# Kernel optimization log

Hardware: AMD Instinct MI355X
Metric: run time of the kernel (lower is better)

Reference implementation:

```python
import jax, jax.numpy as jnp
import numpy as np

T, N, E = 8, 5000, 160000
IN_DIM, HID, H = 64, 128, 8
D = HID // H  # head dim = 16
NC = 2
EPS = 1e-5


def layer_norm(x, g, b):
    mu = jnp.mean(x, axis=-1, keepdims=True)
    var = jnp.mean((x - mu) ** 2, axis=-1, keepdims=True)
    return (x - mu) / jnp.sqrt(var + EPS) * g + b


def setup_inputs() -> dict:
    key = jax.random.key(0)
    ks = jax.random.split(key, 24)
    p = {}
    p["x"] = jax.random.normal(ks[0], (T, N, IN_DIM), dtype=jnp.float32)
    p["edge_index"] = jax.random.randint(ks[1], (T, 2, E), 0, N, dtype=jnp.int32)
    p["noise"] = jax.random.normal(ks[2], (N, HID), dtype=jnp.float32)
    def w(k, shape, fan_in):
        return jax.random.normal(k, shape, dtype=jnp.float32) * (1.0 / np.sqrt(fan_in))
    p["W_proj"] = w(ks[3], (IN_DIM, HID), IN_DIM)
    p["b_proj"] = jnp.zeros((HID,), jnp.float32)
    p["W_gat"] = w(ks[4], (HID, HID), HID)
    p["a_src"] = w(ks[5], (H, D), D)
    p["a_dst"] = w(ks[6], (H, D), D)
    p["b_gat"] = jnp.zeros((HID,), jnp.float32)
    p["g1"] = jnp.ones((HID,), jnp.float32)
    p["be1"] = jnp.zeros((HID,), jnp.float32)
    p["W_qkv"] = w(ks[7], (3 * HID, HID), HID)
    p["b_qkv"] = jnp.zeros((3 * HID,), jnp.float32)
    p["W_o"] = w(ks[8], (HID, HID), HID)
    p["b_o"] = jnp.zeros((HID,), jnp.float32)
    p["g2"] = jnp.ones((HID,), jnp.float32)
    p["be2"] = jnp.zeros((HID,), jnp.float32)
    p["Wc1"] = w(ks[9], (HID, HID), HID)
    p["bc1"] = jnp.zeros((HID,), jnp.float32)
    p["gc"] = jnp.ones((HID,), jnp.float32)
    p["bec"] = jnp.zeros((HID,), jnp.float32)
    p["Wc2"] = w(ks[10], (HID, NC), HID)
    p["bc2"] = jnp.array([0.0, 0.1], jnp.float32)
    return p


def reference(x, edge_index, noise, W_proj, b_proj, W_gat, a_src, a_dst, b_gat,
              g1, be1, W_qkv, b_qkv, W_o, b_o, g2, be2,
              Wc1, bc1, gc, bec, Wc2, bc2):
    # per-timestep projection + ReLU: [T, N, HID]
    h = jax.nn.relu(x @ W_proj + b_proj)

    loop = jnp.arange(N, dtype=edge_index.dtype)

    def gat(h_t, ei):  # h_t: [N, HID], ei: [2, E]
        src = jnp.concatenate([ei[0], loop])  # add self loops
        dst = jnp.concatenate([ei[1], loop])
        xh = (h_t @ W_gat).reshape(N, H, D)          # [N, H, D]
        a_s = jnp.sum(xh * a_src, axis=-1)           # [N, H]
        a_d = jnp.sum(xh * a_dst, axis=-1)           # [N, H]
        e = jax.nn.leaky_relu(a_s[src] + a_d[dst], 0.2)  # [E', H]
        m = jax.ops.segment_max(e, dst, num_segments=N)
        ex = jnp.exp(e - m[dst])
        s = jax.ops.segment_sum(ex, dst, num_segments=N)
        alpha = ex / (s[dst] + 1e-16)                # segment softmax per dst/head
        out = jax.ops.segment_sum(xh[src] * alpha[..., None], dst, num_segments=N)
        return out.reshape(N, HID) + b_gat

    feats = jax.vmap(gat)(h, edge_index)             # [T, N, HID]
    nf = jnp.transpose(feats, (1, 0, 2))             # [N, T, HID] (node = batch)

    nrm = layer_norm(nf, g1, be1)
    qkv = nrm @ W_qkv.T + b_qkv                      # [N, T, 3*HID]
    q, k, v = jnp.split(qkv, 3, axis=-1)
    def heads(t):
        return t.reshape(N, T, H, D).transpose(0, 2, 1, 3)  # [N, H, T, D]
    q, k, v = heads(q), heads(k), heads(v)
    scores = jnp.einsum('nhqd,nhkd->nhqk', q, k) / jnp.sqrt(jnp.float32(D))
    attn = jax.nn.softmax(scores, axis=-1)
    ta = jnp.einsum('nhqk,nhkd->nhqd', attn, v)
    ta = ta.transpose(0, 2, 1, 3).reshape(N, T, HID) @ W_o.T + b_o

    fused = layer_norm(nf + ta, g2, be2)
    emb = fused[:, -1, :]                            # [N, HID]

    node_ids = jnp.arange(N, dtype=jnp.float32) / N
    div = jnp.sin(node_ids * 6.28) * 0.1             # [N]
    emb = emb + div[:, None] + noise * 0.05          # eval noise scale

    h1 = emb @ Wc1 + bc1
    h1 = jax.nn.gelu(layer_norm(h1, gc, bec), approximate=False)
    logits = h1 @ Wc2 + bc2                          # [N, 2]
    sinu = jnp.sin(jnp.arange(N, dtype=jnp.float32) * 0.5) * 0.2
    logits = logits.at[:, 1].add(sinu)
    return emb, logits
```

## Files before the change

### kernel.cpp

```cpp
#include <hip/hip_runtime.h>
#include <math.h>

#define T 8
#define N 5000
#define E 160000
#define EN (E + N)
#define IN_DIM 64
#define HID 128
#define H 8
#define D 16
#define NC 2
#define MT 32
#define NBF 4
#define NRR 8
#define NCHK 32
#define NHCH 32
#define RSZ ((N + NRR - 1) / NRR)
#define CSZ ((EN + NCHK - 1) / NCHK)

__device__ __forceinline__ float leaky(float e) { return (e >= 0.0f) ? e : 0.2f * e; }

__global__ __launch_bounds__(256) void k_pg(const float* __restrict__ x,
                                            const float* __restrict__ Wp,
                                            const float* __restrict__ bp,
                                            const float* __restrict__ Wg,
                                            const float* __restrict__ asrc,
                                            const float* __restrict__ adst,
                                            float* __restrict__ xh,
                                            float* __restrict__ a_s,
                                            float* __restrict__ a_d,
                                            int* __restrict__ cursor) {
    __shared__ float xt[MT][IN_DIM];
    __shared__ float ht[MT][HID + 1];
    int row0 = blockIdx.x * MT;
    int tid = threadIdx.x;

    {
        int gi = blockIdx.x * 256 + tid;
        if (gi < T * N) cursor[gi] = 0;
    }

    for (int idx = tid; idx < MT * IN_DIM; idx += 256) {
        int r = idx >> 6, k = idx & 63;
        xt[r][k] = x[(size_t)(row0 + r) * IN_DIM + k];
    }
    __syncthreads();

    int cg = tid & 31;
    int rg = tid >> 5;
    int c0 = cg * 4, r0 = rg * 4;

    {
        float4 b4 = *(const float4*)(bp + c0);
        float a00=b4.x,a01=b4.y,a02=b4.z,a03=b4.w;
        float a10=b4.x,a11=b4.y,a12=b4.z,a13=b4.w;
        float a20=b4.x,a21=b4.y,a22=b4.z,a23=b4.w;
        float a30=b4.x,a31=b4.y,a32=b4.z,a33=b4.w;
        for (int k = 0; k < IN_DIM; ++k) {
            float4 w = *(const float4*)(Wp + (size_t)k * HID + c0);
            float x0 = xt[r0 + 0][k], x1 = xt[r0 + 1][k];
            float x2 = xt[r0 + 2][k], x3 = xt[r0 + 3][k];
            a00 += x0*w.x; a01 += x0*w.y; a02 += x0*w.z; a03 += x0*w.w;
            a10 += x1*w.x; a11 += x1*w.y; a12 += x1*w.z; a13 += x1*w.w;
            a20 += x2*w.x; a21 += x2*w.y; a22 += x2*w.z; a23 += x2*w.w;
            a30 += x3*w.x; a31 += x3*w.y; a32 += x3*w.z; a33 += x3*w.w;
        }
        ht[r0+0][c0+0]=fmaxf(a00,0.f); ht[r0+0][c0+1]=fmaxf(a01,0.f);
        ht[r0+0][c0+2]=fmaxf(a02,0.f); ht[r0+0][c0+3]=fmaxf(a03,0.f);
        ht[r0+1][c0+0]=fmaxf(a10,0.f); ht[r0+1][c0+1]=fmaxf(a11,0.f);
        ht[r0+1][c0+2]=fmaxf(a12,0.f); ht[r0+1][c0+3]=fmaxf(a13,0.f);
        ht[r0+2][c0+0]=fmaxf(a20,0.f); ht[r0+2][c0+1]=fmaxf(a21,0.f);
        ht[r0+2][c0+2]=fmaxf(a22,0.f); ht[r0+2][c0+3]=fmaxf(a23,0.f);
        ht[r0+3][c0+0]=fmaxf(a30,0.f); ht[r0+3][c0+1]=fmaxf(a31,0.f);
        ht[r0+3][c0+2]=fmaxf(a32,0.f); ht[r0+3][c0+3]=fmaxf(a33,0.f);
    }
    __syncthreads();

    float a00=0,a01=0,a02=0,a03=0, a10=0,a11=0,a12=0,a13=0;
    float a20=0,a21=0,a22=0,a23=0, a30=0,a31=0,a32=0,a33=0;
    for (int k = 0; k < HID; ++k) {
        float4 w = *(const float4*)(Wg + (size_t)k * HID + c0);
        float h0 = ht[r0 + 0][k], h1 = ht[r0 + 1][k];
        float h2 = ht[r0 + 2][k], h3 = ht[r0 + 3][k];
        a00 += h0*w.x; a01 += h0*w.y; a02 += h0*w.z; a03 += h0*w.w;
        a10 += h1*w.x; a11 += h1*w.y; a12 += h1*w.z; a13 += h1*w.w;
        a20 += h2*w.x; a21 += h2*w.y; a22 += h2*w.z; a23 += h2*w.w;
        a30 += h3*w.x; a31 += h3*w.y; a32 += h3*w.z; a33 += h3*w.w;
    }
    {
        float4 v;
        v.x=a00; v.y=a01; v.z=a02; v.w=a03;
        *(float4*)(xh + (size_t)(row0 + r0 + 0) * HID + c0) = v;
        v.x=a10; v.y=a11; v.z=a12; v.w=a13;
        *(float4*)(xh + (size_t)(row0 + r0 + 1) * HID + c0) = v;
        v.x=a20; v.y=a21; v.z=a22; v.w=a23;
        *(float4*)(xh + (size_t)(row0 + r0 + 2) * HID + c0) = v;
        v.x=a30; v.y=a31; v.z=a32; v.w=a33;
        *(float4*)(xh + (size_t)(row0 + r0 + 3) * HID + c0) = v;
    }
    __syncthreads();
    ht[r0+0][c0+0]=a00; ht[r0+0][c0+1]=a01; ht[r0+0][c0+2]=a02; ht[r0+0][c0+3]=a03;
    ht[r0+1][c0+0]=a10; ht[r0+1][c0+1]=a11; ht[r0+1][c0+2]=a12; ht[r0+1][c0+3]=a13;
    ht[r0+2][c0+0]=a20; ht[r0+2][c0+1]=a21; ht[r0+2][c0+2]=a22; ht[r0+2][c0+3]=a23;
    ht[r0+3][c0+0]=a30; ht[r0+3][c0+1]=a31; ht[r0+3][c0+2]=a32; ht[r0+3][c0+3]=a33;
    __syncthreads();

    {
        int r = tid >> 3, hh = tid & 7;
        float s1 = 0.0f, s2 = 0.0f;
        #pragma unroll
        for (int d = 0; d < D; ++d) {
            float v = ht[r][hh * D + d];
            s1 += v * asrc[hh * D + d];
            s2 += v * adst[hh * D + d];
        }
        a_s[(size_t)(row0 + r) * H + hh] = s1;
        a_d[(size_t)(row0 + r) * H + hh] = s2;
    }
}

__global__ void k_tr(const float* __restrict__ W_qkv, const float* __restrict__ W_o,
                     float* __restrict__ WTq, float* __restrict__ WoT) {
    int idx = blockIdx.x * 256 + threadIdx.x;
    if (idx < 384 * 128) {
        int j = idx >> 7, c = idx & 127;
        WTq[c * 384 + j] = W_qkv[idx];
    } else if (idx < 384 * 128 + 128 * 128) {
        int r = idx - 384 * 128;
        int j = r >> 7, k = r & 127;
        WoT[k * 128 + j] = W_o[r];
    }
}

__global__ __launch_bounds__(256) void k_hist(const int* __restrict__ ei,
                                              int* __restrict__ cursor) {
    __shared__ int hist[N];
    int t = blockIdx.x >> 5;
    int chunk = blockIdx.x & 31;
    int tid = threadIdx.x;

    for (int i = tid; i < N; i += 256) hist[i] = 0;
    __syncthreads();

    const int CS = (EN + NHCH - 1) / NHCH;
    int i0 = chunk * CS;
    int i1 = (i0 + CS < EN) ? i0 + CS : EN;
    const int* drow = ei + (size_t)(2 * t + 1) * E;
    for (int i = i0 + tid; i < i1; i += 256) {
        int d = (i < E) ? drow[i] : (i - E);
        atomicAdd(&hist[d], 1);
    }
    __syncthreads();

    int* cur = cursor + t * N;
    for (int i = tid; i < N; i += 256) {
        int c = hist[i];
        if (c) atomicAdd(&cur[i], c);
    }
}

__global__ void k_scan(int* __restrict__ cursor, int* __restrict__ offs) {
    __shared__ int part[256];
    int t = blockIdx.x;
    int tid = threadIdx.x;
    const int CH = 20;
    int begin = tid * CH;
    int sum = 0;
    for (int k = 0; k < CH; ++k) {
        int i = begin + k;
        if (i < N) sum += cursor[t * N + i];
    }
    part[tid] = sum;
    __syncthreads();
    if (tid == 0) {
        int run = 0;
        for (int i = 0; i < 256; ++i) { int v = part[i]; part[i] = run; run += v; }
        offs[t * (N + 1) + N] = run;
    }
    __syncthreads();
    int run = part[tid];
    for (int k = 0; k < CH; ++k) {
        int i = begin + k;
        if (i < N) {
            int cnt = cursor[t * N + i];
            offs[t * (N + 1) + i] = run;
            cursor[t * N + i] = run;
            run += cnt;
        }
    }
}

__global__ __launch_bounds__(256) void k_scatter(const int* __restrict__ ei,
                                                 int* __restrict__ cursor,
                                                 int* __restrict__ csr_src) {
    int idx = blockIdx.x;
    int g = idx & 63;
    int c = idx >> 6;
    int t = g >> 3;
    int r = g & 7;
    int lo = r * RSZ;
    int hi = (lo + RSZ < N) ? lo + RSZ : N;
    int i0 = c * CSZ;
    int i1 = (i0 + CSZ < EN) ? i0 + CSZ : EN;

    const int* srow = ei + (size_t)(2 * t) * E;
    const int* drow = srow + E;
    int* cur = cursor + t * N;
    int* csb = csr_src + (size_t)t * EN;

    for (int i = i0 + threadIdx.x; i < i1; i += 256) {
        int s, d;
        if (i < E) { d = drow[i]; s = srow[i]; }
        else       { s = d = i - E; }
        if (d >= lo && d < hi) {
            int pos = atomicAdd(&cur[d], 1);
            csb[pos] = s;
        }
    }
}

__global__ __launch_bounds__(128) void k_aggc(
        const int* __restrict__ offs, const int* __restrict__ csr_src,
        const float* __restrict__ a_s, const float* __restrict__ a_d,
        const float* __restrict__ xh, const float* __restrict__ b_gat,
        const float* __restrict__ g1, const float* __restrict__ be1,
        float* __restrict__ nrm, float* __restrict__ xlast_g) {
    int b = blockIdx.x;
    int t = b & 7;
    int dst = b >> 3;
    int tid = threadIdx.x;

    int o0 = offs[t * (N + 1) + dst];
    int o1 = offs[t * (N + 1) + dst + 1];
    int deg = o1 - o0;
    const int* esrc = csr_src + (size_t)t * EN + o0;
    const float* as_b = a_s + (size_t)t * N * H;
    const float* ad_b = a_d + (size_t)t * N * H;
    const float* xh_b = xh + (size_t)t * N * HID;

    __shared__ float ws_s[2][H];
    __shared__ float pacc[2][HID];
    __shared__ float red[128];

    int el = tid >> 5;
    int cg = tid & 31;
    int hg = cg >> 2;
    float adh = ad_b[dst * H + hg];

    float4 acc = {0.0f, 0.0f, 0.0f, 0.0f};
    float wpart = 0.0f;

    #pragma unroll 4
    for (int ej = el; ej < deg; ej += 4) {
        int src = esrc[ej];
        float w = expf(leaky(as_b[src * H + hg] + adh));
        wpart += w;
        float4 v = *(const float4*)(xh_b + (size_t)src * HID + (cg << 2));
        acc.x += w * v.x; acc.y += w * v.y;
        acc.z += w * v.z; acc.w += w * v.w;
    }

    wpart += __shfl_xor(wpart, 32);
    acc.x += __shfl_xor(acc.x, 32);
    acc.y += __shfl_xor(acc.y, 32);
    acc.z += __shfl_xor(acc.z, 32);
    acc.w += __shfl_xor(acc.w, 32);
    if (!(tid & 32)) {
        if ((cg & 3) == 0) ws_s[tid >> 6][hg] = wpart;
        *(float4*)&pacc[tid >> 6][cg << 2] = acc;
    }
    __syncthreads();

    float wsum = ws_s[0][tid >> 4] + ws_s[1][tid >> 4];
    float val = (pacc[0][tid] + pacc[1][tid]) / (wsum + 1e-16f);

    float v = val + b_gat[tid];
    red[tid] = v;
    __syncthreads();
    if (tid < 64) {
        float s = red[tid] + red[tid + 64];
        #pragma unroll
        for (int m = 1; m < 64; m <<= 1) s += __shfl_xor(s, m);
        if (tid == 0) red[0] = s;
    }
    __syncthreads();
    float mu = red[0] * (1.0f / HID);
    __syncthreads();
    float dv = v - mu;
    red[tid] = dv * dv;
    __syncthreads();
    if (tid < 64) {
        float s = red[tid] + red[tid + 64];
        #pragma unroll
        for (int m = 1; m < 64; m <<= 1) s += __shfl_xor(s, m);
        if (tid == 0) red[0] = s;
    }
    __syncthreads();
    float rstd = rsqrtf(red[0] * (1.0f / HID) + 1e-5f);

    nrm[(size_t)(dst * T + t) * HID + tid] = dv * rstd * g1[tid] + be1[tid];
    if (t == T - 1) xlast_g[(size_t)dst * HID + tid] = v;
}

__global__ __launch_bounds__(256) void k_fuse(
        const float* __restrict__ nrm,
        const float* __restrict__ WTq,
        const float* __restrict__ b_qkv,
        const float* __restrict__ xlast_g,
        const float* __restrict__ WoT,
        const float* __restrict__ b_o,
        const float* __restrict__ g2, const float* __restrict__ be2,
        const float* __restrict__ noise, float* __restrict__ out) {
    __shared__ float at[NBF * T][HID];
    __shared__ float ql[NBF][HID];
    __shared__ float ws[2][8][384];
    float* ta_s = &at[0][0];

    int n0 = blockIdx.x * NBF;
    int tid = threadIdx.x;
    int cg = tid & 31, rg = tid >> 5;
    int c0 = cg * 4, r0 = rg * 4;
    int u = rg >> 1;
    int lane = tid & 63, wv = tid >> 6;

    auto stage = [&](int kc, int buf) {
        const float* g = WTq + (size_t)kc * 3072 + wv * 768 + (lane << 2);
        float* l = &ws[buf][0][0] + wv * 768;
        #pragma unroll
        for (int j = 0; j < 3; ++j) {
            __builtin_amdgcn_global_load_lds(
                (const __attribute__((address_space(1))) void*)(g + j * 256),
                (__attribute__((address_space(3))) void*)(l + j * 256),
                16, 0, 0);
        }
    };

    {
        const float* srcp = nrm + (size_t)n0 * T * HID;
        for (int idx = tid; idx < NBF * T * 32; idx += 256) {
            int r = idx >> 5, c4 = (idx & 31) << 2;
            *(float4*)&at[r][c4] = *(const float4*)(srcp + (size_t)r * HID + c4);
        }
    }
    stage(0, 0);

    float ka[4][4], va[4][4], qa[4];
    {
        float4 bk = *(const float4*)(b_qkv + 128 + c0);
        float4 bv = *(const float4*)(b_qkv + 256 + c0);
        #pragma unroll
        for (int i = 0; i < 4; ++i) {
            ka[i][0] = bk.x; ka[i][1] = bk.y; ka[i][2] = bk.z; ka[i][3] = bk.w;
            va[i][0] = bv.x; va[i][1] = bv.y; va[i][2] = bv.z; va[i][3] = bv.w;
        }
        if (rg < 4) {
            float4 bq = *(const float4*)(b_qkv + c0);
            qa[0] = bq.x; qa[1] = bq.y; qa[2] = bq.z; qa[3] = bq.w;
        } else {
            qa[0] = qa[1] = qa[2] = qa[3] = 0.0f;
        }
    }
    __syncthreads();

    const float* atq = at[(rg & 3) * T + (T - 1)];

    int cur = 0;
    for (int kc = 0; kc < 16; ++kc) {
        if (kc < 15) stage(kc + 1, cur ^ 1);

        #pragma unroll
        for (int kk = 0; kk < 8; kk += 4) {
            int k = kc * 8 + kk;
            float4 e0 = *(const float4*)&at[r0 + 0][k];
            float4 e1 = *(const float4*)&at[r0 + 1][k];
            float4 e2 = *(const float4*)&at[r0 + 2][k];
            float4 e3 = *(const float4*)&at[r0 + 3][k];
            float e0a[4] = {e0.x, e0.y, e0.z, e0.w};
            float e1a[4] = {e1.x, e1.y, e1.z, e1.w};
            float e2a[4] = {e2.x, e2.y, e2.z, e2.w};
            float e3a[4] = {e3.x, e3.y, e3.z, e3.w};
            float eqa[4] = {0.f, 0.f, 0.f, 0.f};
            if (rg < 4) {
                float4 eq = *(const float4*)&atq[k];
                eqa[0] = eq.x; eqa[1] = eq.y; eqa[2] = eq.z; eqa[3] = eq.w;
            }
            #pragma unroll
            for (int j = 0; j < 4; ++j) {
                float4 wk = *(const float4*)&ws[cur][kk + j][128 + c0];
                float4 wv4 = *(const float4*)&ws[cur][kk + j][256 + c0];
                float x0 = e0a[j], x1 = e1a[j], x2 = e2a[j], x3 = e3a[j];
                ka[0][0] += x0*wk.x; ka[0][1] += x0*wk.y; ka[0][2] += x0*wk.z; ka[0][3] += x0*wk.w;
                ka[1][0] += x1*wk.x; ka[1][1] += x1*wk.y; ka[1][2] += x1*wk.z; ka[1][3] += x1*wk.w;
                ka[2][0] += x2*wk.x; ka[2][1] += x2*wk.y; ka[2][2] += x2*wk.z; ka[2][3] += x2*wk.w;
                ka[3][0] += x3*wk.x; ka[3][1] += x3*wk.y; ka[3][2] += x3*wk.z; ka[3][3] += x3*wk.w;
                va[0][0] += x0*wv4.x; va[0][1] += x0*wv4.y; va[0][2] += x0*wv4.z; va[0][3] += x0*wv4.w;
                va[1][0] += x1*wv4.x; va[1][1] += x1*wv4.y; va[1][2] += x1*wv4.z; va[1][3] += x1*wv4.w;
                va[2][0] += x2*wv4.x; va[2][1] += x2*wv4.y; va[2][2] += x2*wv4.z; va[2][3] += x2*wv4.w;
                va[3][0] += x3*wv4.x; va[3][1] += x3*wv4.y; va[3][2] += x3*wv4.z; va[3][3] += x3*wv4.w;
                if (rg < 4) {
                    float4 wq = *(const float4*)&ws[cur][kk + j][c0];
                    float xq = eqa[j];
                    qa[0] += xq*wq.x; qa[1] += xq*wq.y; qa[2] += xq*wq.z; qa[3] += xq*wq.w;
                }
            }
        }
        __syncthreads();
        cur ^= 1;
    }

    if (rg < 4) {
        float4 q4; q4.x = qa[0]; q4.y = qa[1]; q4.z = qa[2]; q4.w = qa[3];
        *(float4*)&ql[rg][c0] = q4;
    }
    __syncthreads();

    float p0, p1, p2, p3;
    {
        float4 q4 = *(const float4*)&ql[u][c0];
        float ps[4];
        #pragma unroll
        for (int i = 0; i < 4; ++i) {
            float s = q4.x * ka[i][0] + q4.y * ka[i][1]
                    + q4.z * ka[i][2] + q4.w * ka[i][3];
            s += __shfl_xor(s, 1);
            s += __shfl_xor(s, 2);
            ps[i] = s * 0.25f;
        }
        float mx = fmaxf(fmaxf(ps[0], ps[1]), fmaxf(ps[2], ps[3]));
        mx = fmaxf(mx, __shfl_xor(mx, 32));
        float e0 = expf(ps[0] - mx), e1 = expf(ps[1] - mx);
        float e2 = expf(ps[2] - mx), e3 = expf(ps[3] - mx);
        float ssum = e0 + e1 + e2 + e3;
        ssum += __shfl_xor(ssum, 32);
        float inv = 1.0f / ssum;
        p0 = (e0 * va[0][0] + e1 * va[1][0] + e2 * va[2][0] + e3 * va[3][0]) * inv;
        p1 = (e0 * va[0][1] + e1 * va[1][1] + e2 * va[2][1] + e3 * va[3][1]) * inv;
        p2 = (e0 * va[0][2] + e1 * va[1][2] + e2 * va[2][2] + e3 * va[3][2]) * inv;
        p3 = (e0 * va[0][3] + e1 * va[1][3] + e2 * va[2][3] + e3 * va[3][3]) * inv;
        p0 += __shfl_xor(p0, 32);
        p1 += __shfl_xor(p1, 32);
        p2 += __shfl_xor(p2, 32);
        p3 += __shfl_xor(p3, 32);
    }
    if (!(tid & 32)) {
        float4 t4; t4.x = p0; t4.y = p1; t4.z = p2; t4.w = p3;
        *(float4*)&ta_s[u * 128 + c0] = t4;
    }
    __syncthreads();

    {
        int uu = tid >> 6, c = tid & 63;
        int n = n0 + uu;
        float o0 = b_o[c], o1 = b_o[c + 64];
        const float* tar = ta_s + uu * 128;
        #pragma unroll 8
        for (int k = 0; k < HID; k += 4) {
            float t0 = tar[k], t1 = tar[k+1], t2 = tar[k+2], t3 = tar[k+3];
            o0 += t0 * WoT[(size_t)(k+0)*128 + c]  + t1 * WoT[(size_t)(k+1)*128 + c]
                + t2 * WoT[(size_t)(k+2)*128 + c]  + t3 * WoT[(size_t)(k+3)*128 + c];
            o1 += t0 * WoT[(size_t)(k+0)*128 + c+64] + t1 * WoT[(size_t)(k+1)*128 + c+64]
                + t2 * WoT[(size_t)(k+2)*128 + c+64] + t3 * WoT[(size_t)(k+3)*128 + c+64];
        }
        float xa = xlast_g[(size_t)n * HID + c];
        float xb = xlast_g[(size_t)n * HID + c + 64];
        float x2a = xa + o0, x2b = xb + o1;
        float s = x2a + x2b, qs = x2a * x2a + x2b * x2b;
        #pragma unroll
        for (int m = 1; m < 64; m <<= 1) {
            s  += __shfl_xor(s, m);
            qs += __shfl_xor(qs, m);
        }
        float mu = s * (1.0f / HID);
        float var = qs * (1.0f / HID) - mu * mu;
        float rstd = rsqrtf(var + 1e-5f);
        float dv = sinf(((float)n / (float)N) * 6.28f) * 0.1f;
        out[(size_t)n * HID + c] =
            (x2a - mu) * rstd * g2[c] + be2[c] + dv
            + noise[(size_t)n * HID + c] * 0.05f;
        out[(size_t)n * HID + c + 64] =
            (x2b - mu) * rstd * g2[c + 64] + be2[c + 64] + dv
            + noise[(size_t)n * HID + c + 64] * 0.05f;
    }
}

__global__ __launch_bounds__(256) void k_cls(const float* __restrict__ emb,
                                             const float* __restrict__ Wc1,
                                             const float* __restrict__ bc1,
                                             const float* __restrict__ gc,
                                             const float* __restrict__ bec,
                                             const float* __restrict__ Wc2,
                                             const float* __restrict__ bc2,
                                             float* __restrict__ out) {
    __shared__ float et[MT][HID];
    __shared__ float h1t[MT][HID + 1];
    int row0 = blockIdx.x * MT;
    int tid = threadIdx.x;

    for (int idx = tid; idx < MT * HID; idx += 256) {
        int r = idx >> 7, c = idx & 127;
        int row = row0 + r;
        et[r][c] = (row < N) ? emb[(size_t)row * HID + c] : 0.0f;
    }
    __syncthreads();

    {
        int cg = tid & 31, rg = tid >> 5;
        int c0 = cg * 4, r0 = rg * 4;
        float4 b4 = *(const float4*)(bc1 + c0);
        float a00=b4.x,a01=b4.y,a02=b4.z,a03=b4.w;
        float a10=b4.x,a11=b4.y,a12=b4.z,a13=b4.w;
        float a20=b4.x,a21=b4.y,a22=b4.z,a23=b4.w;
        float a30=b4.x,a31=b4.y,a32=b4.z,a33=b4.w;
        for (int k = 0; k < HID; ++k) {
            float4 w = *(const float4*)(Wc1 + (size_t)k * HID + c0);
            float e0 = et[r0 + 0][k], e1 = et[r0 + 1][k];
            float e2 = et[r0 + 2][k], e3 = et[r0 + 3][k];
            a00 += e0*w.x; a01 += e0*w.y; a02 += e0*w.z; a03 += e0*w.w;
            a10 += e1*w.x; a11 += e1*w.y; a12 += e1*w.z; a13 += e1*w.w;
            a20 += e2*w.x; a21 += e2*w.y; a22 += e2*w.z; a23 += e2*w.w;
            a30 += e3*w.x; a31 += e3*w.y; a32 += e3*w.z; a33 += e3*w.w;
        }
        h1t[r0+0][c0+0]=a00; h1t[r0+0][c0+1]=a01; h1t[r0+0][c0+2]=a02; h1t[r0+0][c0+3]=a03;
        h1t[r0+1][c0+0]=a10; h1t[r0+1][c0+1]=a11; h1t[r0+1][c0+2]=a12; h1t[r0+1][c0+3]=a13;
        h1t[r0+2][c0+0]=a20; h1t[r0+2][c0+1]=a21; h1t[r0+2][c0+2]=a22; h1t[r0+2][c0+3]=a23;
        h1t[r0+3][c0+0]=a30; h1t[r0+3][c0+1]=a31; h1t[r0+3][c0+2]=a32; h1t[r0+3][c0+3]=a33;
    }
    __syncthreads();

    {
        int r = tid >> 3, l = tid & 7;
        float p = 0.0f;
        #pragma unroll
        for (int k = 0; k < 16; ++k) p += h1t[r][l + 8 * k];
        #pragma unroll
        for (int m = 1; m < 8; m <<= 1) p += __shfl_xor(p, m);
        float mu = p * (1.0f / HID);
        float v = 0.0f;
        #pragma unroll
        for (int k = 0; k < 16; ++k) { float d = h1t[r][l + 8 * k] - mu; v += d * d; }
        #pragma unroll
        for (int m = 1; m < 8; m <<= 1) v += __shfl_xor(v, m);
        float rstd = rsqrtf(v * (1.0f / HID) + 1e-5f);
        #pragma unroll
        for (int k = 0; k < 16; ++k) {
            int c = l + 8 * k;
            float lnv = (h1t[r][c] - mu) * rstd * gc[c] + bec[c];
            h1t[r][c] = 0.5f * lnv * (1.0f + erff(lnv * 0.70710678118f));
        }
    }
    __syncthreads();

    if (tid < MT * NC) {
        int r = tid >> 1, j = tid & 1;
        int row = row0 + r;
        if (row < N) {
            float acc = bc2[j];
            #pragma unroll 8
            for (int c = 0; c < HID; ++c) acc += h1t[r][c] * Wc2[c * NC + j];
            if (j == 1) acc += sinf((float)row * 0.5f) * 0.2f;
            out[(size_t)N * HID + (size_t)row * NC + j] = acc;
        }
    }
}

extern "C" void kernel_launch(void* const* d_in, const int* in_sizes, int n_in,
                              void* d_out, int out_size, void* d_ws, size_t ws_size,
                              hipStream_t stream) {
    const float* x      = (const float*)d_in[0];
    const int*   ei     = (const int*)d_in[1];
    const float* noise  = (const float*)d_in[2];
    const float* W_proj = (const float*)d_in[3];
    const float* b_proj = (const float*)d_in[4];
    const float* W_gat  = (const float*)d_in[5];
    const float* a_src  = (const float*)d_in[6];
    const float* a_dst  = (const float*)d_in[7];
    const float* b_gat  = (const float*)d_in[8];
    const float* g1     = (const float*)d_in[9];
    const float* be1    = (const float*)d_in[10];
    const float* W_qkv  = (const float*)d_in[11];
    const float* b_qkv  = (const float*)d_in[12];
    const float* W_o    = (const float*)d_in[13];
    const float* b_o    = (const float*)d_in[14];
    const float* g2     = (const float*)d_in[15];
    const float* be2    = (const float*)d_in[16];
    const float* Wc1    = (const float*)d_in[17];
    const float* bc1    = (const float*)d_in[18];
    const float* gc     = (const float*)d_in[19];
    const float* bec    = (const float*)d_in[20];
    const float* Wc2    = (const float*)d_in[21];
    const float* bc2    = (const float*)d_in[22];
    float* out = (float*)d_out;

    float* xh     = (float*)d_ws;
    float* nrm    = xh + 5120000;
    float* a_s    = nrm + 5120000;
    float* a_d    = a_s + 320000;
    int*   offs    = (int*)(a_d + 320000);
    int*   cursor  = offs + 40008;
    int*   csr_src = cursor + 40000;
    float* WTq    = (float*)(csr_src + 1320000);
    float* WoT    = WTq + 49152;
    float* xlastg = WoT + 16384;

    k_tr<<<(384 * 128 + 128 * 128 + 255) / 256, 256, 0, stream>>>(W_qkv, W_o, WTq, WoT);

    k_pg<<<T * N / MT, 256, 0, stream>>>(x, W_proj, b_proj, W_gat, a_src, a_dst,
                                         xh, a_s, a_d, cursor);

    k_hist<<<T * NHCH, 256, 0, stream>>>(ei, cursor);
    k_scan<<<T, 256, 0, stream>>>(cursor, offs);
    k_scatter<<<64 * NCHK, 256, 0, stream>>>(ei, cursor, csr_src);

    k_aggc<<<T * N, 128, 0, stream>>>(offs, csr_src, a_s, a_d, xh,
                                      b_gat, g1, be1, nrm, xlastg);

    k_fuse<<<N / NBF, 256, 0, stream>>>(nrm, WTq, b_qkv, xlastg, WoT, b_o,
                                        g2, be2, noise, out);

    k_cls<<<(N + MT - 1) / MT, 256, 0, stream>>>(out, Wc1, bc1, gc, bec, Wc2, bc2, out);
}
```

Before: 349.6 us.

## Merge weight transpose, projection and edge histogram into one front kernel

Three independent front-stage kernels (weight transpose, projection+GAT linear, destination histogram) are combined into a single launch whose blocks branch on block index into the three roles, sharing a union shared-memory buffer. The cursor zeroing that k_pg used to do is replaced with a hipMemsetAsync before the launch, since histogram blocks now run concurrently with the former zeroing blocks. This removes two launches and lets the atomic histogram overlap the GEMM work. In exchange, every block reserves the largest shared-memory footprint, which may lower occupancy for the transpose and projection blocks, and a memset node is added.

```diff
diff --git a/kernel.cpp b/kernel.cpp
--- a/kernel.cpp
+++ b/kernel.cpp
@@ -18,27 +18,74 @@
 #define RSZ ((N + NRR - 1) / NRR)
 #define CSZ ((EN + NCHK - 1) / NCHK)
 
+#define NB_HIST (T * NHCH)
+#define NB_TR   256
+#define NB_PG   (T * N / MT)
+
 __device__ __forceinline__ float leaky(float e) { return (e >= 0.0f) ? e : 0.2f * e; }
 
-__global__ __launch_bounds__(256) void k_pg(const float* __restrict__ x,
-                                            const float* __restrict__ Wp,
-                                            const float* __restrict__ bp,
-                                            const float* __restrict__ Wg,
-                                            const float* __restrict__ asrc,
-                                            const float* __restrict__ adst,
-                                            float* __restrict__ xh,
-                                            float* __restrict__ a_s,
-                                            float* __restrict__ a_d,
-                                            int* __restrict__ cursor) {
-    __shared__ float xt[MT][IN_DIM];
-    __shared__ float ht[MT][HID + 1];
-    int row0 = blockIdx.x * MT;
+__global__ __launch_bounds__(256) void k_front(
+        const float* __restrict__ x,
+        const float* __restrict__ Wp,
+        const float* __restrict__ bp,
+        const float* __restrict__ Wg,
+        const float* __restrict__ asrc,
+        const float* __restrict__ adst,
+        float* __restrict__ xh,
+        float* __restrict__ a_s,
+        float* __restrict__ a_d,
+        const float* __restrict__ W_qkv,
+        const float* __restrict__ W_o,
+        float* __restrict__ WTq,
+        float* __restrict__ WoT,
+        const int* __restrict__ ei,
+        int* __restrict__ cursor) {
+    __shared__ float smem[6272];
+    int bid = blockIdx.x;
     int tid = threadIdx.x;
 
-    {
-        int gi = blockIdx.x * 256 + tid;
-        if (gi < T * N) cursor[gi] = 0;
-    }
+    if (bid < NB_HIST) {
+        int* hist = (int*)smem;
+        int t = bid >> 5;
+        int chunk = bid & 31;
+
+        for (int i = tid; i < N; i += 256) hist[i] = 0;
+        __syncthreads();
+
+        const int CS = (EN + NHCH - 1) / NHCH;
+        int i0 = chunk * CS;
+        int i1 = (i0 + CS < EN) ? i0 + CS : EN;
+        const int* drow = ei + (size_t)(2 * t + 1) * E;
+        for (int i = i0 + tid; i < i1; i += 256) {
+            int d = (i < E) ? drow[i] : (i - E);
+            atomicAdd(&hist[d], 1);
+        }
+        __syncthreads();
+
+        int* cur = cursor + t * N;
+        for (int i = tid; i < N; i += 256) {
+            int c = hist[i];
+            if (c) atomicAdd(&cur[i], c);
+        }
+        return;
+    }
+
+    if (bid < NB_HIST + NB_TR) {
+        int idx = (bid - NB_HIST) * 256 + tid;
+        if (idx < 384 * 128) {
+            int j = idx >> 7, c = idx & 127;
+            WTq[c * 384 + j] = W_qkv[idx];
+        } else if (idx < 384 * 128 + 128 * 128) {
+            int r = idx - 384 * 128;
+            int j = r >> 7, k = r & 127;
+            WoT[k * 128 + j] = W_o[r];
+        }
+        return;
+    }
+
+    float (*xt)[IN_DIM] = (float (*)[IN_DIM])smem;
+    float (*ht)[HID + 1] = (float (*)[HID + 1])(smem + MT * IN_DIM);
+    int row0 = (bid - NB_HIST - NB_TR) * MT;
 
     for (int idx = tid; idx < MT * IN_DIM; idx += 256) {
         int r = idx >> 6, k = idx & 63;
@@ -116,46 +163,6 @@
         }
         a_s[(size_t)(row0 + r) * H + hh] = s1;
         a_d[(size_t)(row0 + r) * H + hh] = s2;
-    }
-}
-
-__global__ void k_tr(const float* __restrict__ W_qkv, const float* __restrict__ W_o,
-                     float* __restrict__ WTq, float* __restrict__ WoT) {
-    int idx = blockIdx.x * 256 + threadIdx.x;
-    if (idx < 384 * 128) {
-        int j = idx >> 7, c = idx & 127;
-        WTq[c * 384 + j] = W_qkv[idx];
-    } else if (idx < 384 * 128 + 128 * 128) {
-        int r = idx - 384 * 128;
-        int j = r >> 7, k = r & 127;
-        WoT[k * 128 + j] = W_o[r];
-    }
-}
-
-__global__ __launch_bounds__(256) void k_hist(const int* __restrict__ ei,
-                                              int* __restrict__ cursor) {
-    __shared__ int hist[N];
-    int t = blockIdx.x >> 5;
-    int chunk = blockIdx.x & 31;
-    int tid = threadIdx.x;
-
-    for (int i = tid; i < N; i += 256) hist[i] = 0;
-    __syncthreads();
-
-    const int CS = (EN + NHCH - 1) / NHCH;
-    int i0 = chunk * CS;
-    int i1 = (i0 + CS < EN) ? i0 + CS : EN;
-    const int* drow = ei + (size_t)(2 * t + 1) * E;
-    for (int i = i0 + tid; i < i1; i += 256) {
-        int d = (i < E) ? drow[i] : (i - E);
-        atomicAdd(&hist[d], 1);
-    }
-    __syncthreads();
-
-    int* cur = cursor + t * N;
-    for (int i = tid; i < N; i += 256) {
-        int c = hist[i];
-        if (c) atomicAdd(&cur[i], c);
     }
 }
 
@@ -602,12 +609,12 @@
     float* WoT    = WTq + 49152;
     float* xlastg = WoT + 16384;
 
-    k_tr<<<(384 * 128 + 128 * 128 + 255) / 256, 256, 0, stream>>>(W_qkv, W_o, WTq, WoT);
-
-    k_pg<<<T * N / MT, 256, 0, stream>>>(x, W_proj, b_proj, W_gat, a_src, a_dst,
-                                         xh, a_s, a_d, cursor);
-
-    k_hist<<<T * NHCH, 256, 0, stream>>>(ei, cursor);
+    hipMemsetAsync(cursor, 0, 40000 * sizeof(int), stream);
+
+    k_front<<<NB_HIST + NB_TR + NB_PG, 256, 0, stream>>>(
+        x, W_proj, b_proj, W_gat, a_src, a_dst, xh, a_s, a_d,
+        W_qkv, W_o, WTq, WoT, ei, cursor);
+
     k_scan<<<T, 256, 0, stream>>>(cursor, offs);
     k_scatter<<<64 * NCHK, 256, 0, stream>>>(ei, cursor, csr_src);
 
```

Result: faster. 341.7 us, median of 2 (-2.3%).
